# Optimization experiments

Hardware: AMD Instinct MI355X
Metric: run time of the kernel (lower is better)

The kernel has to match this reference:

```python
import jax, jax.numpy as jnp
import numpy as np

N = 100_000      # nodes
E = 1_600_000    # edges (no self loops; reference appends them)
G = 1_000        # graphs
FIN = 27         # input node features
HID = 128        # hidden_channels
L = 4            # num_layers
H = 8            # num_heads
B = 4            # num_bases
A = 3            # aggregators: sum, mean, max
FH = HID // H    # per-head out dim
EPS = 1e-5


def setup_inputs() -> dict:
    key = jax.random.key(0)
    ks = jax.random.split(key, 16)
    s = 0.05
    x = jax.random.normal(ks[0], (N, FIN), jnp.float32)
    src = jax.random.randint(ks[1], (E,), 0, N)
    off = jax.random.randint(ks[2], (E,), 1, N)
    dst = (src + off) % N  # guaranteed no self loops
    edge_index = jnp.stack([src, dst]).astype(jnp.int64)
    batch = jnp.sort(jax.random.randint(ks[3], (N,), 0, G)).astype(jnp.int64)
    return {
        "x": x,
        "lin1_w": jax.random.normal(ks[4], (FIN, HID), jnp.float32) * s,
        "lin1_b": jnp.zeros((HID,), jnp.float32),
        "bn1_g": jnp.ones((HID,), jnp.float32),
        "bn1_b": jnp.zeros((HID,), jnp.float32),
        "bases_w": jax.random.normal(ks[5], (L, HID, B * FH), jnp.float32) * s,
        "comb_w": jax.random.normal(ks[6], (L, HID, H * B * A), jnp.float32) * s,
        "comb_b": jnp.zeros((L, H * B * A), jnp.float32),
        "conv_bias": jnp.zeros((L, HID), jnp.float32),
        "bn_g": jnp.ones((L, HID), jnp.float32),
        "bn_b": jnp.zeros((L, HID), jnp.float32),
        "mlp_w1": jax.random.normal(ks[7], (HID, HID // 2), jnp.float32) * s,
        "mbn1_g": jnp.ones((HID // 2,), jnp.float32),
        "mbn1_b": jnp.zeros((HID // 2,), jnp.float32),
        "mlp_w2": jax.random.normal(ks[8], (HID // 2, HID // 4), jnp.float32) * s,
        "mbn2_g": jnp.ones((HID // 4,), jnp.float32),
        "mbn2_b": jnp.zeros((HID // 4,), jnp.float32),
        "mlp_w3": jax.random.normal(ks[9], (HID // 4, 10), jnp.float32) * s,
        "mlp_b3": jnp.zeros((10,), jnp.float32),
        "edge_index": edge_index,
        "batch": batch,
    }


def _bn(h, g, b):
    # BatchNorm1d, training mode (biased batch variance), per-feature over nodes
    mu = jnp.mean(h, axis=0)
    var = jnp.mean((h - mu) ** 2, axis=0)
    return g * (h - mu) * jax.lax.rsqrt(var + EPS) + b


def reference(x, lin1_w, lin1_b, bn1_g, bn1_b, bases_w, comb_w, comb_b,
              conv_bias, bn_g, bn_b, mlp_w1, mbn1_g, mbn1_b, mlp_w2,
              mbn2_g, mbn2_b, mlp_w3, mlp_b3, edge_index, batch):
    # add self loops (inputs contain none, matching remove+add in EGConv)
    loop = jnp.arange(N, dtype=edge_index.dtype)
    src = jnp.concatenate([edge_index[0], loop])
    dst = jnp.concatenate([edge_index[1], loop])

    h = jax.nn.relu(_bn(x @ lin1_w + lin1_b, bn1_g, bn1_b))  # [N, HID]

    ones_e = jnp.ones((src.shape[0], 1), h.dtype)
    deg = jax.ops.segment_sum(ones_e, dst, num_segments=N)  # [N,1], >=1 via self loops

    for l in range(L):
        bases = h @ bases_w[l]                              # [N, B*FH]
        comb = (h @ comb_w[l] + comb_b[l]).reshape(N, H, A * B)
        msg = bases[src]                                    # [E+N, B*FH]
        ssum = jax.ops.segment_sum(msg, dst, num_segments=N)
        smean = ssum / deg
        smax = jax.ops.segment_max(msg, dst, num_segments=N)
        agg = jnp.stack([ssum, smean, smax], axis=1)        # [N, A, B*FH]
        agg = agg.reshape(N, A * B, FH)
        out = jnp.einsum('nhk,nkf->nhf', comb, agg).reshape(N, HID) + conv_bias[l]
        h = h + jax.nn.relu(_bn(out, bn_g[l], bn_b[l]))

    # global mean pool over graphs
    gsum = jax.ops.segment_sum(h, batch, num_segments=G)
    gcnt = jnp.maximum(jax.ops.segment_sum(jnp.ones((N, 1), h.dtype), batch, num_segments=G), 1.0)
    g = gsum / gcnt                                         # [G, HID]

    g = jax.nn.relu(_bn(g @ mlp_w1, mbn1_g, mbn1_b))
    g = jax.nn.relu(_bn(g @ mlp_w2, mbn2_g, mbn2_b))
    return g @ mlp_w3 + mlp_b3                              # [G, 10]
```

## Files before the change

### kernel.cpp

```cpp
#include <hip/hip_runtime.h>

#define EPSV 1e-5f
#define NEGINF -3.402823466e38f
#define NBMAX 1600
#define CHUNK 8192
#define CAP3 6144

typedef short bf16x8 __attribute__((ext_vector_type(8)));
typedef float f32x4 __attribute__((ext_vector_type(4)));

__device__ __forceinline__ unsigned short f2bf(float f) {
    union { float f; unsigned i; } c; c.f = f;
    unsigned r = c.i + 0x7fff + ((c.i >> 16) & 1);
    return (unsigned short)(r >> 16);
}
__device__ __forceinline__ float blo(unsigned u) {
    union { unsigned i; float f; } c; c.i = u << 16; return c.f;
}
__device__ __forceinline__ float bhi(unsigned u) {
    union { unsigned i; float f; } c; c.i = u & 0xffff0000u; return c.f;
}
__device__ __forceinline__ float bfu(unsigned short u) {
    union { unsigned i; float f; } c; c.i = ((unsigned)u) << 16; return c.f;
}

__global__ __launch_bounds__(256)
void k_lin1(const float* __restrict__ x, const float* __restrict__ w,
            const float* __restrict__ bvec, unsigned short* __restrict__ outb,
            float* __restrict__ stats, int N)
{
    __shared__ float wl[27 * 128];
    int tid = threadIdx.x;
    for (int i = tid; i < 27 * 128; i += 256) wl[i] = w[i];
    __syncthreads();

    int l  = tid & 63;
    int wv = tid >> 6;
    float bv0 = bvec[l], bv1 = bvec[64 + l];
    int waveSlots = gridDim.x * 4;
    int trips = (N + waveSlots - 1) / waveSlots;
    float s0 = 0.f, q0 = 0.f, s1 = 0.f, q1 = 0.f;
    for (int it = 0; it < trips; ++it) {
        int n = (it * gridDim.x + blockIdx.x) * 4 + wv;
        if (n < N) {
            const float* xr = x + (size_t)n * 27;
            float a0 = bv0, a1 = bv1;
            #pragma unroll
            for (int k = 0; k < 27; ++k) {
                float xv = xr[k];
                a0 = fmaf(xv, wl[k * 128 + l], a0);
                a1 = fmaf(xv, wl[k * 128 + 64 + l], a1);
            }
            outb[(size_t)n * 128 + l] = f2bf(a0);
            outb[(size_t)n * 128 + 64 + l] = f2bf(a1);
            s0 += a0; q0 += a0 * a0; s1 += a1; q1 += a1 * a1;
        }
    }
    __shared__ float sred[4][256];
    sred[0][tid] = s0; sred[1][tid] = q0;
    sred[2][tid] = s1; sred[3][tid] = q1;
    __syncthreads();
    if (tid < 64) {
        int t = tid;
        float v0 = sred[0][t] + sred[0][t + 64] + sred[0][t + 128] + sred[0][t + 192];
        float v1 = sred[1][t] + sred[1][t + 64] + sred[1][t + 128] + sred[1][t + 192];
        float v2 = sred[2][t] + sred[2][t + 64] + sred[2][t + 128] + sred[2][t + 192];
        float v3 = sred[3][t] + sred[3][t + 64] + sred[3][t + 128] + sred[3][t + 192];
        atomicAdd(stats + t, v0);
        atomicAdd(stats + 128 + t, v1);
        atomicAdd(stats + 64 + t, v2);
        atomicAdd(stats + 192 + t, v3);
    }
}

__global__ __launch_bounds__(256)
void k_p1_hist(const int* __restrict__ dst, int* __restrict__ bcnt,
               int E, int NB, int shift)
{
    __shared__ int hist[NBMAX];
    for (int i = threadIdx.x; i < NB; i += 256) hist[i] = 0;
    __syncthreads();
    int stride = gridDim.x * 256;
    for (int e = blockIdx.x * 256 + threadIdx.x; e < E; e += stride)
        atomicAdd(&hist[dst[e] >> shift], 1);
    __syncthreads();
    for (int i = threadIdx.x; i < NB; i += 256)
        if (hist[i]) atomicAdd(bcnt + i, hist[i]);
}

__global__ void k_scan1(const int* __restrict__ cnt, int* __restrict__ rowptr,
                        int* __restrict__ bsum, int N)
{
    __shared__ int sb[256];
    int i = blockIdx.x * 256 + threadIdx.x;
    int v = (i < N) ? cnt[i] : 0;
    sb[threadIdx.x] = v;
    __syncthreads();
    for (int ofs = 1; ofs < 256; ofs <<= 1) {
        int u = (threadIdx.x >= ofs) ? sb[threadIdx.x - ofs] : 0;
        __syncthreads();
        sb[threadIdx.x] += u;
        __syncthreads();
    }
    if (i < N) rowptr[i] = sb[threadIdx.x] - v;
    if (threadIdx.x == 255) bsum[blockIdx.x] = sb[255];
}

__global__ void k_scan2(int* __restrict__ bs, int nb)
{
    __shared__ int sb[512];
    int t = threadIdx.x;
    int v = (t < nb) ? bs[t] : 0;
    sb[t] = v;
    __syncthreads();
    for (int ofs = 1; ofs < 512; ofs <<= 1) {
        int u = (t >= ofs) ? sb[t - ofs] : 0;
        __syncthreads();
        sb[t] += u;
        __syncthreads();
    }
    bs[t] = sb[t] - v;
}

__global__ void k_scan3(int* __restrict__ rowptr, const int* __restrict__ bsum,
                        int N, int E)
{
    int i = blockIdx.x * blockDim.x + threadIdx.x;
    if (i < N) rowptr[i] += bsum[i >> 8];
    if (i == 0) rowptr[N] = E;
}

__global__ __launch_bounds__(256)
void k_p2_scatter(const int* __restrict__ src, const int* __restrict__ dst,
                  const int* __restrict__ bbase, int* __restrict__ bcur0,
                  uint2* __restrict__ bucketed, int E, int NB, int shift)
{
    __shared__ uint2 ebuf[CHUNK];
    __shared__ int hist[NBMAX];
    __shared__ int cur[NBMAX];
    __shared__ int wtmp[256];
    int tid = threadIdx.x;
    int c0 = blockIdx.x * CHUNK;
    int cc = min(CHUNK, E - c0);
    if (cc <= 0) return;

    for (int i = tid; i < NB; i += 256) hist[i] = 0;
    __syncthreads();
    for (int i = tid; i < cc; i += 256)
        atomicAdd(&hist[dst[c0 + i] >> shift], 1);
    __syncthreads();
    int per = (NB + 255) / 256;
    int beg = tid * per, end = min(beg + per, NB);
    int s = 0;
    for (int i = beg; i < end; ++i) s += hist[i];
    wtmp[tid] = s;
    __syncthreads();
    for (int ofs = 1; ofs < 256; ofs <<= 1) {
        int u = (tid >= ofs) ? wtmp[tid - ofs] : 0;
        __syncthreads();
        wtmp[tid] += u;
        __syncthreads();
    }
    int run = wtmp[tid] - s;
    for (int i = beg; i < end; ++i) { cur[i] = run; run += hist[i]; }
    __syncthreads();
    for (int i = tid; i < cc; i += 256) {
        int sv = src[c0 + i], dv = dst[c0 + i];
        int b = dv >> shift;
        int pos = atomicAdd(&cur[b], 1);
        ebuf[pos] = make_uint2((unsigned)sv, (unsigned)dv);
    }
    __syncthreads();
    for (int b = tid; b < NB; b += 256) {
        int c = hist[b];
        if (c > 0) {
            int lb = cur[b] - c;
            int gb = bbase[b] + atomicAdd(&bcur0[b], c);
            hist[b] = gb - lb;
        }
    }
    __syncthreads();
    for (int i = tid; i < cc; i += 256) {
        uint2 u = ebuf[i];
        int b = (int)(u.y >> shift);
        bucketed[hist[b] + i] = u;
    }
}

__global__ __launch_bounds__(256)
void k_p3_csr(const uint2* __restrict__ bucketed, const int* __restrict__ bbase,
              int* __restrict__ rowptr, int* __restrict__ csr,
              int N, int NB, int shift)
{
    __shared__ int ncnt[128], nsc[128];
    __shared__ int lcsr[CAP3];
    int b = blockIdx.x;
    int tid = threadIdx.x;
    int e0 = bbase[b], e1 = bbase[b + 1];
    int cnt = e1 - e0;
    int node0 = b << shift;
    int nodes = min(1 << shift, N - node0);

    if (tid < 128) ncnt[tid] = 0;
    __syncthreads();
    for (int i = tid; i < cnt; i += 256)
        atomicAdd(&ncnt[(int)bucketed[e0 + i].y - node0], 1);
    __syncthreads();
    if (tid < 128) nsc[tid] = ncnt[tid];
    __syncthreads();
    for (int ofs = 1; ofs < 128; ofs <<= 1) {
        int u = 0;
        if (tid < 128 && tid >= ofs) u = nsc[tid - ofs];
        __syncthreads();
        if (tid < 128) nsc[tid] += u;
        __syncthreads();
    }
    if (tid < nodes) rowptr[node0 + tid] = e0 + nsc[tid] - ncnt[tid];
    if (tid == 0 && b == NB - 1) rowptr[N] = e1;
    if (tid < 128) ncnt[tid] = nsc[tid] - ncnt[tid];
    __syncthreads();
    if (cnt <= CAP3) {
        for (int i = tid; i < cnt; i += 256) {
            uint2 u = bucketed[e0 + i];
            int d = (int)u.y - node0;
            int pos = atomicAdd(&ncnt[d], 1);
            lcsr[pos] = (int)u.x;
        }
        __syncthreads();
        for (int i = tid; i < cnt; i += 256) csr[e0 + i] = lcsr[i];
    } else {
        for (int i = tid; i < cnt; i += 256) {
            uint2 u = bucketed[e0 + i];
            int d = (int)u.y - node0;
            int pos = atomicAdd(&ncnt[d], 1);
            csr[e0 + pos] = (int)u.x;
        }
    }
}

__global__ __launch_bounds__(256)
void k_gemm_mfma(const unsigned short* __restrict__ tin, unsigned short* __restrict__ h,
                 const float* __restrict__ stats, const float* __restrict__ gamma,
                 const float* __restrict__ beta, float invN, int residual,
                 const float* __restrict__ basesW, const float* __restrict__ combW,
                 const float* __restrict__ combB,
                 unsigned short* __restrict__ basesP,
                 unsigned short* __restrict__ combB16, int N)
{
    __shared__ unsigned short Wlds[2560 * 8];
    __shared__ float scL[128], shL[128];
    int tid = threadIdx.x;
    if (tid < 128) {
        float mu  = stats[tid] * invN;
        float var = stats[128 + tid] * invN - mu * mu;
        float sc  = gamma[tid] * rsqrtf(var + EPSV);
        scL[tid] = sc;
        shL[tid] = beta[tid] - mu * sc;
    }
    for (int i = tid; i < 2560; i += 256) {
        int ct = i >> 8, rem = i & 255;
        int ln = rem & 63;
        int n16 = ln & 15, quad = ln >> 4;
        int k = ((rem >> 6) << 5) + quad * 8;
        unsigned short tmp[8];
        if (ct < 4) {
            int c = ct * 16 + n16;
            #pragma unroll
            for (int j = 0; j < 8; ++j) tmp[j] = f2bf(basesW[(k + j) * 64 + c]);
        } else {
            int c = (ct - 4) * 16 + n16;
            #pragma unroll
            for (int j = 0; j < 8; ++j) tmp[j] = f2bf(combW[(k + j) * 96 + c]);
        }
        uint4 pk;
        pk.x = (unsigned)tmp[0] | ((unsigned)tmp[1] << 16);
        pk.y = (unsigned)tmp[2] | ((unsigned)tmp[3] << 16);
        pk.z = (unsigned)tmp[4] | ((unsigned)tmp[5] << 16);
        pk.w = (unsigned)tmp[6] | ((unsigned)tmp[7] << 16);
        *(uint4*)&Wlds[(size_t)i * 8] = pk;
    }
    __syncthreads();

    int lane = tid & 63, wv = tid >> 6;
    int f = lane & 15, quad = lane >> 4;
    float cbv[6];
    #pragma unroll
    for (int s = 0; s < 6; ++s) cbv[s] = combB[s * 16 + f];

    int tiles = (N + 15) >> 4;
    int waveSlots = gridDim.x * 4;
    for (int tile = blockIdx.x * 4 + wv; tile < tiles; tile += waveSlots) {
        int tb = tile * 16;
        int mnode = min(tb + f, N - 1);
        size_t rbase = (size_t)mnode * 128;

        f32x4 acc[10];
        #pragma unroll
        for (int ct = 0; ct < 10; ++ct) acc[ct] = (f32x4){0.f, 0.f, 0.f, 0.f};

        #pragma unroll
        for (int ki = 0; ki < 4; ++ki) {
            int kc = quad * 8 + ki * 32;
            uint4 tv = *(const uint4*)&tin[rbase + kc];
            float r0, r1, r2, r3, r4, r5, r6, r7;
            r0 = fmaxf(blo(tv.x) * scL[kc]     + shL[kc],     0.f);
            r1 = fmaxf(bhi(tv.x) * scL[kc + 1] + shL[kc + 1], 0.f);
            r2 = fmaxf(blo(tv.y) * scL[kc + 2] + shL[kc + 2], 0.f);
            r3 = fmaxf(bhi(tv.y) * scL[kc + 3] + shL[kc + 3], 0.f);
            r4 = fmaxf(blo(tv.z) * scL[kc + 4] + shL[kc + 4], 0.f);
            r5 = fmaxf(bhi(tv.z) * scL[kc + 5] + shL[kc + 5], 0.f);
            r6 = fmaxf(blo(tv.w) * scL[kc + 6] + shL[kc + 6], 0.f);
            r7 = fmaxf(bhi(tv.w) * scL[kc + 7] + shL[kc + 7], 0.f);
            if (residual) {
                uint4 hv = *(const uint4*)&h[rbase + kc];
                r0 += blo(hv.x); r1 += bhi(hv.x); r2 += blo(hv.y); r3 += bhi(hv.y);
                r4 += blo(hv.z); r5 += bhi(hv.z); r6 += blo(hv.w); r7 += bhi(hv.w);
            }
            unsigned short b0 = f2bf(r0), b1 = f2bf(r1), b2 = f2bf(r2), b3 = f2bf(r3);
            unsigned short b4 = f2bf(r4), b5 = f2bf(r5), b6 = f2bf(r6), b7 = f2bf(r7);
            uint4 hw;
            hw.x = (unsigned)b0 | ((unsigned)b1 << 16);
            hw.y = (unsigned)b2 | ((unsigned)b3 << 16);
            hw.z = (unsigned)b4 | ((unsigned)b5 << 16);
            hw.w = (unsigned)b6 | ((unsigned)b7 << 16);
            *(uint4*)&h[rbase + kc] = hw;
            short ab[8] = {(short)b0, (short)b1, (short)b2, (short)b3,
                           (short)b4, (short)b5, (short)b6, (short)b7};
            bf16x8 a = *(bf16x8*)ab;
            #pragma unroll
            for (int ct = 0; ct < 10; ++ct) {
                bf16x8 bfr = *(const bf16x8*)&Wlds[(size_t)((ct * 4 + ki) * 64 + lane) * 8];
                acc[ct] = __builtin_amdgcn_mfma_f32_16x16x32_bf16(a, bfr, acc[ct], 0, 0, 0);
            }
        }

        #pragma unroll
        for (int r = 0; r < 4; ++r) {
            int node = tb + quad * 4 + r;
            if (node < N) {
                #pragma unroll
                for (int ct = 0; ct < 4; ++ct)
                    basesP[(size_t)node * 64 + f * 4 + ct] = f2bf(acc[ct][r]);
                #pragma unroll
                for (int s = 0; s < 6; ++s)
                    combB16[(size_t)node * 96 + s * 16 + f] = f2bf(acc[4 + s][r] + cbv[s]);
            }
        }
    }
}

__global__ __launch_bounds__(256)
void k_agg(const unsigned short* __restrict__ basesP, const unsigned short* __restrict__ combB16,
           const int* __restrict__ csr, const int* __restrict__ rowptr,
           const float* __restrict__ cbias, unsigned short* __restrict__ outb,
           float* __restrict__ stats, int N)
{
    int l = threadIdx.x & 63;
    int w = threadIdx.x >> 6;
    int f = l & 15, sub = l >> 4;
    const char* bp = (const char*)basesP;
    unsigned fof = (unsigned)(f << 3);
    float cb0 = cbias[l], cb1 = cbias[64 + l];
    int waveSlots = gridDim.x * 4;
    int pairs = (N + 1) >> 1;
    int trips = (pairs + waveSlots - 1) / waveSlots;
    float s0 = 0.f, q0 = 0.f, s1 = 0.f, q1 = 0.f;

    for (int it = 0; it < trips; ++it) {
        int pr = (it * gridDim.x + blockIdx.x) * 4 + w;
        if (pr < pairs) {
            int nA = pr * 2;
            bool hasB = (nA + 1) < N;
            int nB = hasB ? nA + 1 : nA;
            int rA = rowptr[nA];
            int cA = rowptr[nA + 1] - rA;
            int rB = rowptr[nB];
            int cB = hasB ? (rowptr[nB + 1] - rB) : 0;

            float SA0 = 0.f, SA1 = 0.f, SA2 = 0.f, SA3 = 0.f;
            float MA0 = NEGINF, MA1 = NEGINF, MA2 = NEGINF, MA3 = NEGINF;
            float SB0 = 0.f, SB1 = 0.f, SB2 = 0.f, SB3 = 0.f;
            float MB0 = NEGINF, MB1 = NEGINF, MB2 = NEGINF, MB3 = NEGINF;

            int mt = (max(cA, cB) + 3) >> 2;
            int e = sub;
            #pragma unroll 2
            for (int t = 0; t < mt; ++t) {
                int eA = max(min(e, cA - 1), 0);
                int eB = max(min(e, cB - 1), 0);
                int snA = csr[rA + eA];
                int snB = csr[rB + eB];
                uint2 uA = *(const uint2*)(bp + (((unsigned)snA) << 7) + fof);
                uint2 uB = *(const uint2*)(bp + (((unsigned)snB) << 7) + fof);
                bool vA = e < cA, vB = e < cB;
                float a0 = blo(uA.x), a1 = bhi(uA.x), a2 = blo(uA.y), a3 = bhi(uA.y);
                float b0 = blo(uB.x), b1 = bhi(uB.x), b2 = blo(uB.y), b3 = bhi(uB.y);
                SA0 += vA ? a0 : 0.f; SA1 += vA ? a1 : 0.f;
                SA2 += vA ? a2 : 0.f; SA3 += vA ? a3 : 0.f;
                MA0 = fmaxf(MA0, vA ? a0 : NEGINF); MA1 = fmaxf(MA1, vA ? a1 : NEGINF);
                MA2 = fmaxf(MA2, vA ? a2 : NEGINF); MA3 = fmaxf(MA3, vA ? a3 : NEGINF);
                SB0 += vB ? b0 : 0.f; SB1 += vB ? b1 : 0.f;
                SB2 += vB ? b2 : 0.f; SB3 += vB ? b3 : 0.f;
                MB0 = fmaxf(MB0, vB ? b0 : NEGINF); MB1 = fmaxf(MB1, vB ? b1 : NEGINF);
                MB2 = fmaxf(MB2, vB ? b2 : NEGINF); MB3 = fmaxf(MB3, vB ? b3 : NEGINF);
                e += 4;
            }

            {
                float T0 = SA0, T1 = SA1, T2 = SA2, T3 = SA3;
                float X0 = MA0, X1 = MA1, X2 = MA2, X3 = MA3;
                T0 += __shfl_xor(T0, 16, 64); T1 += __shfl_xor(T1, 16, 64);
                T2 += __shfl_xor(T2, 16, 64); T3 += __shfl_xor(T3, 16, 64);
                T0 += __shfl_xor(T0, 32, 64); T1 += __shfl_xor(T1, 32, 64);
                T2 += __shfl_xor(T2, 32, 64); T3 += __shfl_xor(T3, 32, 64);
                X0 = fmaxf(X0, __shfl_xor(X0, 16, 64)); X1 = fmaxf(X1, __shfl_xor(X1, 16, 64));
                X2 = fmaxf(X2, __shfl_xor(X2, 16, 64)); X3 = fmaxf(X3, __shfl_xor(X3, 16, 64));
                X0 = fmaxf(X0, __shfl_xor(X0, 32, 64)); X1 = fmaxf(X1, __shfl_xor(X1, 32, 64));
                X2 = fmaxf(X2, __shfl_xor(X2, 32, 64)); X3 = fmaxf(X3, __shfl_xor(X3, 32, 64));
                uint2 su = *(const uint2*)(bp + (((unsigned)nA) << 7) + fof);
                float w0 = blo(su.x), w1 = bhi(su.x), w2 = blo(su.y), w3 = bhi(su.y);
                T0 += w0; T1 += w1; T2 += w2; T3 += w3;
                X0 = fmaxf(X0, w0); X1 = fmaxf(X1, w1);
                X2 = fmaxf(X2, w2); X3 = fmaxf(X3, w3);
                float invd = 1.f / (float)(cA + 1);
                float A0 = T0 * invd, A1 = T1 * invd, A2 = T2 * invd, A3 = T3 * invd;

                const unsigned short* cr = combB16 + (size_t)nA * 96;
                const uint2* c0p = (const uint2*)(cr + sub * 12);
                const uint2* c1p = (const uint2*)(cr + 48 + sub * 12);
                uint2 qa0 = c0p[0], qa1 = c0p[1], qa2 = c0p[2];
                uint2 qb0 = c1p[0], qb1 = c1p[1], qb2 = c1p[2];

                float o0 = cb0, o1 = cb1;
                o0 = fmaf(blo(qa0.x), T0, o0); o0 = fmaf(bhi(qa0.x), T1, o0);
                o0 = fmaf(blo(qa0.y), T2, o0); o0 = fmaf(bhi(qa0.y), T3, o0);
                o0 = fmaf(blo(qa1.x), A0, o0); o0 = fmaf(bhi(qa1.x), A1, o0);
                o0 = fmaf(blo(qa1.y), A2, o0); o0 = fmaf(bhi(qa1.y), A3, o0);
                o0 = fmaf(blo(qa2.x), X0, o0); o0 = fmaf(bhi(qa2.x), X1, o0);
                o0 = fmaf(blo(qa2.y), X2, o0); o0 = fmaf(bhi(qa2.y), X3, o0);
                o1 = fmaf(blo(qb0.x), T0, o1); o1 = fmaf(bhi(qb0.x), T1, o1);
                o1 = fmaf(blo(qb0.y), T2, o1); o1 = fmaf(bhi(qb0.y), T3, o1);
                o1 = fmaf(blo(qb1.x), A0, o1); o1 = fmaf(bhi(qb1.x), A1, o1);
                o1 = fmaf(blo(qb1.y), A2, o1); o1 = fmaf(bhi(qb1.y), A3, o1);
                o1 = fmaf(blo(qb2.x), X0, o1); o1 = fmaf(bhi(qb2.x), X1, o1);
                o1 = fmaf(blo(qb2.y), X2, o1); o1 = fmaf(bhi(qb2.y), X3, o1);

                outb[(size_t)nA * 128 + l] = f2bf(o0);
                outb[(size_t)nA * 128 + 64 + l] = f2bf(o1);
                s0 += o0; q0 += o0 * o0; s1 += o1; q1 += o1 * o1;
            }
            if (hasB) {
                float T0 = SB0, T1 = SB1, T2 = SB2, T3 = SB3;
                float X0 = MB0, X1 = MB1, X2 = MB2, X3 = MB3;
                T0 += __shfl_xor(T0, 16, 64); T1 += __shfl_xor(T1, 16, 64);
                T2 += __shfl_xor(T2, 16, 64); T3 += __shfl_xor(T3, 16, 64);
                T0 += __shfl_xor(T0, 32, 64); T1 += __shfl_xor(T1, 32, 64);
                T2 += __shfl_xor(T2, 32, 64); T3 += __shfl_xor(T3, 32, 64);
                X0 = fmaxf(X0, __shfl_xor(X0, 16, 64)); X1 = fmaxf(X1, __shfl_xor(X1, 16, 64));
                X2 = fmaxf(X2, __shfl_xor(X2, 16, 64)); X3 = fmaxf(X3, __shfl_xor(X3, 16, 64));
                X0 = fmaxf(X0, __shfl_xor(X0, 32, 64)); X1 = fmaxf(X1, __shfl_xor(X1, 32, 64));
                X2 = fmaxf(X2, __shfl_xor(X2, 32, 64)); X3 = fmaxf(X3, __shfl_xor(X3, 32, 64));
                uint2 su = *(const uint2*)(bp + (((unsigned)nB) << 7) + fof);
                float w0 = blo(su.x), w1 = bhi(su.x), w2 = blo(su.y), w3 = bhi(su.y);
                T0 += w0; T1 += w1; T2 += w2; T3 += w3;
                X0 = fmaxf(X0, w0); X1 = fmaxf(X1, w1);
                X2 = fmaxf(X2, w2); X3 = fmaxf(X3, w3);
                float invd = 1.f / (float)(cB + 1);
                float A0 = T0 * invd, A1 = T1 * invd, A2 = T2 * invd, A3 = T3 * invd;

                const unsigned short* cr = combB16 + (size_t)nB * 96;
                const uint2* c0p = (const uint2*)(cr + sub * 12);
                const uint2* c1p = (const uint2*)(cr + 48 + sub * 12);
                uint2 qa0 = c0p[0], qa1 = c0p[1], qa2 = c0p[2];
                uint2 qb0 = c1p[0], qb1 = c1p[1], qb2 = c1p[2];

                float o0 = cb0, o1 = cb1;
                o0 = fmaf(blo(qa0.x), T0, o0); o0 = fmaf(bhi(qa0.x), T1, o0);
                o0 = fmaf(blo(qa0.y), T2, o0); o0 = fmaf(bhi(qa0.y), T3, o0);
                o0 = fmaf(blo(qa1.x), A0, o0); o0 = fmaf(bhi(qa1.x), A1, o0);
                o0 = fmaf(blo(qa1.y), A2, o0); o0 = fmaf(bhi(qa1.y), A3, o0);
                o0 = fmaf(blo(qa2.x), X0, o0); o0 = fmaf(bhi(qa2.x), X1, o0);
                o0 = fmaf(blo(qa2.y), X2, o0); o0 = fmaf(bhi(qa2.y), X3, o0);
                o1 = fmaf(blo(qb0.x), T0, o1); o1 = fmaf(bhi(qb0.x), T1, o1);
                o1 = fmaf(blo(qb0.y), T2, o1); o1 = fmaf(bhi(qb0.y), T3, o1);
                o1 = fmaf(blo(qb1.x), A0, o1); o1 = fmaf(bhi(qb1.x), A1, o1);
                o1 = fmaf(blo(qb1.y), A2, o1); o1 = fmaf(bhi(qb1.y), A3, o1);
                o1 = fmaf(blo(qb2.x), X0, o1); o1 = fmaf(bhi(qb2.x), X1, o1);
                o1 = fmaf(blo(qb2.y), X2, o1); o1 = fmaf(bhi(qb2.y), X3, o1);

                outb[(size_t)nB * 128 + l] = f2bf(o0);
                outb[(size_t)nB * 128 + 64 + l] = f2bf(o1);
                s0 += o0; q0 += o0 * o0; s1 += o1; q1 += o1 * o1;
            }
        }
    }
    __shared__ float sred[4][256];
    sred[0][threadIdx.x] = s0; sred[1][threadIdx.x] = q0;
    sred[2][threadIdx.x] = s1; sred[3][threadIdx.x] = q1;
    __syncthreads();
    if (threadIdx.x < 64) {
        int t = threadIdx.x;
        float v0 = sred[0][t] + sred[0][t + 64] + sred[0][t + 128] + sred[0][t + 192];
        float v1 = sred[1][t] + sred[1][t + 64] + sred[1][t + 128] + sred[1][t + 192];
        float v2 = sred[2][t] + sred[2][t + 64] + sred[2][t + 128] + sred[2][t + 192];
        float v3 = sred[3][t] + sred[3][t + 64] + sred[3][t + 128] + sred[3][t + 192];
        atomicAdd(stats + t, v0);
        atomicAdd(stats + 128 + t, v1);
        atomicAdd(stats + 64 + t, v2);
        atomicAdd(stats + 192 + t, v3);
    }
}

__global__ void k_gbound(const int* __restrict__ batch, int* __restrict__ gstart,
                         int N, int G)
{
    int stride = gridDim.x * blockDim.x;
    for (int n = blockIdx.x * blockDim.x + threadIdx.x; n < N; n += stride) {
        int b = batch[n];
        if (n == 0) {
            for (int g = 0; g <= b; ++g) gstart[g] = 0;
        } else {
            int pb = batch[n - 1];
            for (int g = pb + 1; g <= b; ++g) gstart[g] = n;
        }
        if (n == N - 1) {
            for (int g = b + 1; g <= G; ++g) gstart[g] = N;
        }
    }
}

__global__ __launch_bounds__(256)
void k_gmean(const unsigned short* __restrict__ t, const unsigned short* __restrict__ h,
             const float* __restrict__ stats, const float* __restrict__ gamma,
             const float* __restrict__ beta, float invN,
             const int* __restrict__ gstart, float* __restrict__ gout, int G)
{
    __shared__ float part[128];
    int g = blockIdx.x;
    if (g >= G) return;
    int c = threadIdx.x & 127;
    int half = threadIdx.x >> 7;
    float mu  = stats[c] * invN;
    float var = stats[128 + c] * invN - mu * mu;
    float sc  = gamma[c] * rsqrtf(var + EPSV);
    float sh  = beta[c] - mu * sc;
    int s = gstart[g], e = gstart[g + 1];
    float acc = 0.f;
    #pragma unroll 2
    for (int n = s + half; n < e; n += 2) {
        size_t o = (size_t)n * 128 + c;
        acc += bfu(h[o]) + fmaxf(bfu(t[o]) * sc + sh, 0.f);
    }
    if (half) part[c] = acc;
    __syncthreads();
    if (!half) {
        float tot = acc + part[c];
        float cntf = fmaxf((float)(e - s), 1.f);
        gout[g * 128 + c] = tot / cntf;
    }
}

__global__ void k_mlp1(const float* __restrict__ gin, const float* __restrict__ w1,
                       float* __restrict__ t1, float* __restrict__ stats, int G)
{
    int g = blockIdx.x;
    int c = threadIdx.x;
    const float* gr = gin + g * 128;
    float acc = 0.f;
    for (int k = 0; k < 128; ++k) acc = fmaf(gr[k], w1[k * 64 + c], acc);
    t1[g * 64 + c] = acc;
    atomicAdd(stats + c, acc);
    atomicAdd(stats + 64 + c, acc * acc);
}

__global__ void k_mlp2(const float* __restrict__ t1, const float* __restrict__ stats1,
                       const float* __restrict__ g1, const float* __restrict__ b1,
                       const float* __restrict__ w2, float* __restrict__ t2,
                       float* __restrict__ stats2, float invG, int G)
{
    __shared__ float row[64];
    int g = blockIdx.x;
    int c = threadIdx.x;
    float v = t1[g * 64 + c];
    float mu = stats1[c] * invG;
    float var = stats1[64 + c] * invG - mu * mu;
    row[c] = fmaxf(g1[c] * (v - mu) * rsqrtf(var + EPSV) + b1[c], 0.f);
    __syncthreads();
    if (c < 32) {
        float acc = 0.f;
        #pragma unroll
        for (int k = 0; k < 64; ++k) acc = fmaf(row[k], w2[k * 32 + c], acc);
        t2[g * 32 + c] = acc;
        atomicAdd(stats2 + c, acc);
        atomicAdd(stats2 + 32 + c, acc * acc);
    }
}

__global__ void k_mlp3(const float* __restrict__ t2, const float* __restrict__ stats2,
                       const float* __restrict__ g2, const float* __restrict__ b2,
                       const float* __restrict__ w3, const float* __restrict__ b3,
                       float* __restrict__ out, float invG, int G)
{
    __shared__ float row[32];
    int g = blockIdx.x;
    int c = threadIdx.x;
    if (c < 32) {
        float v = t2[g * 32 + c];
        float mu = stats2[c] * invG;
        float var = stats2[32 + c] * invG - mu * mu;
        row[c] = fmaxf(g2[c] * (v - mu) * rsqrtf(var + EPSV) + b2[c], 0.f);
    }
    __syncthreads();
    if (c < 10) {
        float acc = b3[c];
        #pragma unroll
        for (int k = 0; k < 32; ++k) acc = fmaf(row[k], w3[k * 10 + c], acc);
        out[g * 10 + c] = acc;
    }
}

extern "C" void kernel_launch(void* const* d_in, const int* in_sizes, int n_in,
                              void* d_out, int out_size, void* d_ws, size_t ws_size,
                              hipStream_t stream)
{
    const float* x        = (const float*)d_in[0];
    const float* lin1_w   = (const float*)d_in[1];
    const float* lin1_b   = (const float*)d_in[2];
    const float* bn1_g    = (const float*)d_in[3];
    const float* bn1_b    = (const float*)d_in[4];
    const float* bases_w  = (const float*)d_in[5];
    const float* comb_w   = (const float*)d_in[6];
    const float* comb_b   = (const float*)d_in[7];
    const float* conv_bias= (const float*)d_in[8];
    const float* bn_g     = (const float*)d_in[9];
    const float* bn_b     = (const float*)d_in[10];
    const float* mlp_w1   = (const float*)d_in[11];
    const float* mbn1_g   = (const float*)d_in[12];
    const float* mbn1_b   = (const float*)d_in[13];
    const float* mlp_w2   = (const float*)d_in[14];
    const float* mbn2_g   = (const float*)d_in[15];
    const float* mbn2_b   = (const float*)d_in[16];
    const float* mlp_w3   = (const float*)d_in[17];
    const float* mlp_b3   = (const float*)d_in[18];
    const int*   edge_idx = (const int*)d_in[19];
    const int*   batch    = (const int*)d_in[20];
    float* outp = (float*)d_out;

    const int N = in_sizes[20];
    const int E = in_sizes[19] / 2;
    const int G = out_size / 10;
    const int* esrc = edge_idx;
    const int* edst = edge_idx + E;

    int shift = 6;
    while ((((N - 1) >> shift) + 1) > NBMAX && shift < 7) ++shift;
    const int NB = ((N - 1) >> shift) + 1;

    char* p = (char*)d_ws;
    auto alloc = [&](size_t bytes) {
        char* r = p;
        p += (bytes + 255) & ~(size_t)255;
        return r;
    };
    unsigned short* h      = (unsigned short*)alloc((size_t)N * 128 * 2);
    unsigned short* basesP = (unsigned short*)alloc((size_t)N * 64 * 2);
    unsigned short* combB16= (unsigned short*)alloc((size_t)N * 96 * 2);
    unsigned short* outb   = (unsigned short*)alloc((size_t)N * 128 * 2);
    int*            csr    = (int*)  alloc((size_t)(E + 64) * 4);
    int*            rowptr = (int*)  alloc((size_t)(N + 1) * 4);
    int*            bbase  = (int*)  alloc((size_t)(NB + 1) * 4);
    float*          tg     = (float*)alloc((size_t)G * 128 * 4);
    float*          t1     = (float*)alloc((size_t)G * 64 * 4);
    float*          t2     = (float*)alloc((size_t)G * 32 * 4);
    int*            gstart = (int*)  alloc((size_t)(G + 1) * 4);
    int*            bsum   = (int*)  alloc(512 * 4);
    char*           zbase  = p;
    int*            bcnt   = (int*)  alloc((size_t)NB * 4);
    int*            bcur0  = (int*)  alloc((size_t)NB * 4);
    float*          stats  = (float*)alloc(7 * 256 * 4);
    size_t zbytes = (size_t)(p - zbase);
    uint2* bucketed = (uint2*)combB16;
    (void)ws_size; (void)n_in;

    hipMemsetAsync(zbase, 0, zbytes, stream);

    const float invN = 1.0f / (float)N;
    const float invG = 1.0f / (float)G;
    const int nbB = (NB + 255) / 256;

    k_lin1<<<1024, 256, 0, stream>>>(x, lin1_w, lin1_b, outb, stats, N);
    k_p1_hist<<<256, 256, 0, stream>>>(edst, bcnt, E, NB, shift);
    k_scan1<<<nbB, 256, 0, stream>>>(bcnt, bbase, bsum, NB);
    k_scan2<<<1, 512, 0, stream>>>(bsum, nbB);
    k_scan3<<<nbB, 256, 0, stream>>>(bbase, bsum, NB, E);
    k_p2_scatter<<<(E + CHUNK - 1) / CHUNK, 256, 0, stream>>>(esrc, edst, bbase, bcur0,
                                                              bucketed, E, NB, shift);
    k_p3_csr<<<NB, 256, 0, stream>>>(bucketed, bbase, rowptr, csr, N, NB, shift);

    for (int l = 0; l < 4; ++l) {
        const float* bw = bases_w + (size_t)l * 128 * 64;
        const float* cw = comb_w + (size_t)l * 128 * 96;
        const float* cb = comb_b + (size_t)l * 96;
        const float* cvb = conv_bias + (size_t)l * 128;
        const float* pg = (l == 0) ? bn1_g : bn_g + (l - 1) * 128;
        const float* pb = (l == 0) ? bn1_b : bn_b + (l - 1) * 128;
        k_gemm_mfma<<<512, 256, 0, stream>>>(outb, h, stats + l * 256, pg, pb, invN,
                                             l > 0 ? 1 : 0, bw, cw, cb, basesP, combB16, N);
        k_agg<<<2048, 256, 0, stream>>>(basesP, combB16, csr, rowptr, cvb,
                                        outb, stats + (1 + l) * 256, N);
    }

    k_gbound<<<512, 256, 0, stream>>>(batch, gstart, N, G);
    k_gmean<<<G, 256, 0, stream>>>(outb, h, stats + 4 * 256, bn_g + 3 * 128,
                                   bn_b + 3 * 128, invN, gstart, tg, G);
    float* st5 = stats + 5 * 256;
    float* st6 = stats + 6 * 256;
    k_mlp1<<<G, 64, 0, stream>>>(tg, mlp_w1, t1, st5, G);
    k_mlp2<<<G, 64, 0, stream>>>(t1, st5, mbn1_g, mbn1_b, mlp_w2, t2, st6, invG, G);
    k_mlp3<<<G, 64, 0, stream>>>(t2, st6, mbn2_g, mbn2_b, mlp_w3, mlp_b3, outp, invG, G);
}
```

Measured before the change: 778.7 us.

## Fuse histogram+scan+graph-bounds and pooling+MLP tail into last-block kernels

Merges the bucket histogram, the three-kernel scan and the graph-boundary computation into one launch, where the last histogram block to arrive (detected with an atomic counter) performs the exclusive scan. Likewise fuses graph mean pooling and the three MLP/BN stages into one kernel, with the last-arriving block doing the batch-norm-dependent MLP layers 2 and 3 serially. The aggregation kernel's duplicated A/B epilogue is folded into an unrolled loop. This removes about seven kernel launches and their gaps, but puts the tail MLP work on a single block and relies on threadfence/atomic last-block ordering.

Result: slower. 982.5 us (+26.2%).

```diff
diff --git a/kernel.cpp b/kernel.cpp
--- a/kernel.cpp
+++ b/kernel.cpp
@@ -74,60 +74,67 @@
 }
 
 __global__ __launch_bounds__(256)
-void k_p1_hist(const int* __restrict__ dst, int* __restrict__ bcnt,
-               int E, int NB, int shift)
-{
+void k_prep(const int* __restrict__ dst, int* __restrict__ bcnt, int* __restrict__ bbase,
+            int E, int NB, int shift, const int* __restrict__ batch,
+            int* __restrict__ gstart, int N, int G, int* __restrict__ arrive)
+{
+    const int HB = 256;
+    int tid = threadIdx.x;
     __shared__ int hist[NBMAX];
-    for (int i = threadIdx.x; i < NB; i += 256) hist[i] = 0;
-    __syncthreads();
-    int stride = gridDim.x * 256;
-    for (int e = blockIdx.x * 256 + threadIdx.x; e < E; e += stride)
-        atomicAdd(&hist[dst[e] >> shift], 1);
-    __syncthreads();
-    for (int i = threadIdx.x; i < NB; i += 256)
-        if (hist[i]) atomicAdd(bcnt + i, hist[i]);
-}
-
-__global__ void k_scan1(const int* __restrict__ cnt, int* __restrict__ rowptr,
-                        int* __restrict__ bsum, int N)
-{
-    __shared__ int sb[256];
-    int i = blockIdx.x * 256 + threadIdx.x;
-    int v = (i < N) ? cnt[i] : 0;
-    sb[threadIdx.x] = v;
-    __syncthreads();
-    for (int ofs = 1; ofs < 256; ofs <<= 1) {
-        int u = (threadIdx.x >= ofs) ? sb[threadIdx.x - ofs] : 0;
-        __syncthreads();
-        sb[threadIdx.x] += u;
-        __syncthreads();
-    }
-    if (i < N) rowptr[i] = sb[threadIdx.x] - v;
-    if (threadIdx.x == 255) bsum[blockIdx.x] = sb[255];
-}
-
-__global__ void k_scan2(int* __restrict__ bs, int nb)
-{
-    __shared__ int sb[512];
-    int t = threadIdx.x;
-    int v = (t < nb) ? bs[t] : 0;
-    sb[t] = v;
-    __syncthreads();
-    for (int ofs = 1; ofs < 512; ofs <<= 1) {
-        int u = (t >= ofs) ? sb[t - ofs] : 0;
-        __syncthreads();
-        sb[t] += u;
-        __syncthreads();
-    }
-    bs[t] = sb[t] - v;
-}
-
-__global__ void k_scan3(int* __restrict__ rowptr, const int* __restrict__ bsum,
-                        int N, int E)
-{
-    int i = blockIdx.x * blockDim.x + threadIdx.x;
-    if (i < N) rowptr[i] += bsum[i >> 8];
-    if (i == 0) rowptr[N] = E;
+    __shared__ int buf2[NBMAX];
+    __shared__ int partl[256];
+    __shared__ int lastf;
+
+    if (blockIdx.x < HB) {
+        for (int i = tid; i < NB; i += 256) hist[i] = 0;
+        __syncthreads();
+        int stride = HB * 256;
+        for (int e = blockIdx.x * 256 + tid; e < E; e += stride)
+            atomicAdd(&hist[dst[e] >> shift], 1);
+        __syncthreads();
+        for (int i = tid; i < NB; i += 256)
+            if (hist[i]) atomicAdd(bcnt + i, hist[i]);
+        __syncthreads();
+        if (tid == 0) {
+            __threadfence();
+            int tk = atomicAdd(arrive, 1);
+            lastf = (tk == HB - 1) ? 1 : 0;
+        }
+        __syncthreads();
+        if (lastf) {
+            __threadfence();
+            int per = (NB + 255) / 256;
+            int beg = tid * per, end = min(beg + per, NB);
+            int s = 0;
+            for (int i = beg; i < end; ++i) { int v = bcnt[i]; buf2[i] = s; s += v; }
+            partl[tid] = s;
+            __syncthreads();
+            for (int ofs = 1; ofs < 256; ofs <<= 1) {
+                int u = (tid >= ofs) ? partl[tid - ofs] : 0;
+                __syncthreads();
+                partl[tid] += u;
+                __syncthreads();
+            }
+            int add = partl[tid] - s;
+            for (int i = beg; i < end; ++i) bbase[i] = buf2[i] + add;
+            if (tid == 0) bbase[NB] = E;
+        }
+    } else {
+        int b = blockIdx.x - HB;
+        int stride = (gridDim.x - HB) * 256;
+        for (int n = b * 256 + tid; n < N; n += stride) {
+            int bb = batch[n];
+            if (n == 0) {
+                for (int g = 0; g <= bb; ++g) gstart[g] = 0;
+            } else {
+                int pb = batch[n - 1];
+                for (int g = pb + 1; g <= bb; ++g) gstart[g] = n;
+            }
+            if (n == N - 1) {
+                for (int g = bb + 1; g <= G; ++g) gstart[g] = N;
+            }
+        }
+    }
 }
 
 __global__ __launch_bounds__(256)
@@ -406,9 +413,15 @@
                 e += 4;
             }
 
-            {
-                float T0 = SA0, T1 = SA1, T2 = SA2, T3 = SA3;
-                float X0 = MA0, X1 = MA1, X2 = MA2, X3 = MA3;
+            #pragma unroll
+            for (int m = 0; m < 2; ++m) {
+                if (m == 1 && !hasB) break;
+                int n = (m == 0) ? nA : nB;
+                int cnt = (m == 0) ? cA : cB;
+                float T0 = (m == 0) ? SA0 : SB0, T1 = (m == 0) ? SA1 : SB1;
+                float T2 = (m == 0) ? SA2 : SB2, T3 = (m == 0) ? SA3 : SB3;
+                float X0 = (m == 0) ? MA0 : MB0, X1 = (m == 0) ? MA1 : MB1;
+                float X2 = (m == 0) ? MA2 : MB2, X3 = (m == 0) ? MA3 : MB3;
                 T0 += __shfl_xor(T0, 16, 64); T1 += __shfl_xor(T1, 16, 64);
                 T2 += __shfl_xor(T2, 16, 64); T3 += __shfl_xor(T3, 16, 64);
                 T0 += __shfl_xor(T0, 32, 64); T1 += __shfl_xor(T1, 32, 64);
@@ -417,15 +430,15 @@
                 X2 = fmaxf(X2, __shfl_xor(X2, 16, 64)); X3 = fmaxf(X3, __shfl_xor(X3, 16, 64));
                 X0 = fmaxf(X0, __shfl_xor(X0, 32, 64)); X1 = fmaxf(X1, __shfl_xor(X1, 32, 64));
                 X2 = fmaxf(X2, __shfl_xor(X2, 32, 64)); X3 = fmaxf(X3, __shfl_xor(X3, 32, 64));
-                uint2 su = *(const uint2*)(bp + (((unsigned)nA) << 7) + fof);
+                uint2 su = *(const uint2*)(bp + (((unsigned)n) << 7) + fof);
                 float w0 = blo(su.x), w1 = bhi(su.x), w2 = blo(su.y), w3 = bhi(su.y);
                 T0 += w0; T1 += w1; T2 += w2; T3 += w3;
                 X0 = fmaxf(X0, w0); X1 = fmaxf(X1, w1);
                 X2 = fmaxf(X2, w2); X3 = fmaxf(X3, w3);
-                float invd = 1.f / (float)(cA + 1);
+                float invd = 1.f / (float)(cnt + 1);
                 float A0 = T0 * invd, A1 = T1 * invd, A2 = T2 * invd, A3 = T3 * invd;
 
-                const unsigned short* cr = combB16 + (size_t)nA * 96;
+                const unsigned short* cr = combB16 + (size_t)n * 96;
                 const uint2* c0p = (const uint2*)(cr + sub * 12);
                 const uint2* c1p = (const uint2*)(cr + 48 + sub * 12);
                 uint2 qa0 = c0p[0], qa1 = c0p[1], qa2 = c0p[2];
@@ -445,51 +458,8 @@
                 o1 = fmaf(blo(qb2.x), X0, o1); o1 = fmaf(bhi(qb2.x), X1, o1);
                 o1 = fmaf(blo(qb2.y), X2, o1); o1 = fmaf(bhi(qb2.y), X3, o1);
 
-                outb[(size_t)nA * 128 + l] = f2bf(o0);
-                outb[(size_t)nA * 128 + 64 + l] = f2bf(o1);
-                s0 += o0; q0 += o0 * o0; s1 += o1; q1 += o1 * o1;
-            }
-            if (hasB) {
-                float T0 = SB0, T1 = SB1, T2 = SB2, T3 = SB3;
-                float X0 = MB0, X1 = MB1, X2 = MB2, X3 = MB3;
-                T0 += __shfl_xor(T0, 16, 64); T1 += __shfl_xor(T1, 16, 64);
-                T2 += __shfl_xor(T2, 16, 64); T3 += __shfl_xor(T3, 16, 64);
-                T0 += __shfl_xor(T0, 32, 64); T1 += __shfl_xor(T1, 32, 64);
-                T2 += __shfl_xor(T2, 32, 64); T3 += __shfl_xor(T3, 32, 64);
-                X0 = fmaxf(X0, __shfl_xor(X0, 16, 64)); X1 = fmaxf(X1, __shfl_xor(X1, 16, 64));
-                X2 = fmaxf(X2, __shfl_xor(X2, 16, 64)); X3 = fmaxf(X3, __shfl_xor(X3, 16, 64));
-                X0 = fmaxf(X0, __shfl_xor(X0, 32, 64)); X1 = fmaxf(X1, __shfl_xor(X1, 32, 64));
-                X2 = fmaxf(X2, __shfl_xor(X2, 32, 64)); X3 = fmaxf(X3, __shfl_xor(X3, 32, 64));
-                uint2 su = *(const uint2*)(bp + (((unsigned)nB) << 7) + fof);
-                float w0 = blo(su.x), w1 = bhi(su.x), w2 = blo(su.y), w3 = bhi(su.y);
-                T0 += w0; T1 += w1; T2 += w2; T3 += w3;
-                X0 = fmaxf(X0, w0); X1 = fmaxf(X1, w1);
-                X2 = fmaxf(X2, w2); X3 = fmaxf(X3, w3);
-                float invd = 1.f / (float)(cB + 1);
-                float A0 = T0 * invd, A1 = T1 * invd, A2 = T2 * invd, A3 = T3 * invd;
-
-                const unsigned short* cr = combB16 + (size_t)nB * 96;
-                const uint2* c0p = (const uint2*)(cr + sub * 12);
-                const uint2* c1p = (const uint2*)(cr + 48 + sub * 12);
-                uint2 qa0 = c0p[0], qa1 = c0p[1], qa2 = c0p[2];
-                uint2 qb0 = c1p[0], qb1 = c1p[1], qb2 = c1p[2];
-
-                float o0 = cb0, o1 = cb1;
-                o0 = fmaf(blo(qa0.x), T0, o0); o0 = fmaf(bhi(qa0.x), T1, o0);
-                o0 = fmaf(blo(qa0.y), T2, o0); o0 = fmaf(bhi(qa0.y), T3, o0);
-                o0 = fmaf(blo(qa1.x), A0, o0); o0 = fmaf(bhi(qa1.x), A1, o0);
-                o0 = fmaf(blo(qa1.y), A2, o0); o0 = fmaf(bhi(qa1.y), A3, o0);
-                o0 = fmaf(blo(qa2.x), X0, o0); o0 = fmaf(bhi(qa2.x), X1, o0);
-                o0 = fmaf(blo(qa2.y), X2, o0); o0 = fmaf(bhi(qa2.y), X3, o0);
-                o1 = fmaf(blo(qb0.x), T0, o1); o1 = fmaf(bhi(qb0.x), T1, o1);
-                o1 = fmaf(blo(qb0.y), T2, o1); o1 = fmaf(bhi(qb0.y), T3, o1);
-                o1 = fmaf(blo(qb1.x), A0, o1); o1 = fmaf(bhi(qb1.x), A1, o1);
-                o1 = fmaf(blo(qb1.y), A2, o1); o1 = fmaf(bhi(qb1.y), A3, o1);
-                o1 = fmaf(blo(qb2.x), X0, o1); o1 = fmaf(bhi(qb2.x), X1, o1);
-                o1 = fmaf(blo(qb2.y), X2, o1); o1 = fmaf(bhi(qb2.y), X3, o1);
-
-                outb[(size_t)nB * 128 + l] = f2bf(o0);
-                outb[(size_t)nB * 128 + 64 + l] = f2bf(o1);
+                outb[(size_t)n * 128 + l] = f2bf(o0);
+                outb[(size_t)n * 128 + 64 + l] = f2bf(o1);
                 s0 += o0; q0 += o0 * o0; s1 += o1; q1 += o1 * o1;
             }
         }
@@ -511,111 +481,111 @@
     }
 }
 
-__global__ void k_gbound(const int* __restrict__ batch, int* __restrict__ gstart,
-                         int N, int G)
-{
-    int stride = gridDim.x * blockDim.x;
-    for (int n = blockIdx.x * blockDim.x + threadIdx.x; n < N; n += stride) {
-        int b = batch[n];
-        if (n == 0) {
-            for (int g = 0; g <= b; ++g) gstart[g] = 0;
-        } else {
-            int pb = batch[n - 1];
-            for (int g = pb + 1; g <= b; ++g) gstart[g] = n;
-        }
-        if (n == N - 1) {
-            for (int g = b + 1; g <= G; ++g) gstart[g] = N;
-        }
-    }
-}
-
 __global__ __launch_bounds__(256)
-void k_gmean(const unsigned short* __restrict__ t, const unsigned short* __restrict__ h,
-             const float* __restrict__ stats, const float* __restrict__ gamma,
-             const float* __restrict__ beta, float invN,
-             const int* __restrict__ gstart, float* __restrict__ gout, int G)
-{
+void k_tail(const unsigned short* __restrict__ t, const unsigned short* __restrict__ h,
+            const float* __restrict__ stats4, const float* __restrict__ gamma,
+            const float* __restrict__ beta, float invN, const int* __restrict__ gstart,
+            const float* __restrict__ w1, float* __restrict__ t1, float* __restrict__ st5,
+            const float* __restrict__ g1, const float* __restrict__ b1,
+            const float* __restrict__ w2, float* __restrict__ t2,
+            const float* __restrict__ g2, const float* __restrict__ b2,
+            const float* __restrict__ w3, const float* __restrict__ b3,
+            float* __restrict__ out, float invG, int G, int* __restrict__ arrive)
+{
+    __shared__ float tg[128];
     __shared__ float part[128];
+    __shared__ float red[4][64];
+    __shared__ int lastf;
+    __shared__ float sc1[64], sh1[64], s6[64];
+    __shared__ float sc2[32], sh2[32];
+
     int g = blockIdx.x;
-    if (g >= G) return;
-    int c = threadIdx.x & 127;
-    int half = threadIdx.x >> 7;
-    float mu  = stats[c] * invN;
-    float var = stats[128 + c] * invN - mu * mu;
-    float sc  = gamma[c] * rsqrtf(var + EPSV);
-    float sh  = beta[c] - mu * sc;
-    int s = gstart[g], e = gstart[g + 1];
-    float acc = 0.f;
-    #pragma unroll 2
-    for (int n = s + half; n < e; n += 2) {
-        size_t o = (size_t)n * 128 + c;
-        acc += bfu(h[o]) + fmaxf(bfu(t[o]) * sc + sh, 0.f);
-    }
-    if (half) part[c] = acc;
-    __syncthreads();
-    if (!half) {
-        float tot = acc + part[c];
-        float cntf = fmaxf((float)(e - s), 1.f);
-        gout[g * 128 + c] = tot / cntf;
-    }
-}
-
-__global__ void k_mlp1(const float* __restrict__ gin, const float* __restrict__ w1,
-                       float* __restrict__ t1, float* __restrict__ stats, int G)
-{
-    int g = blockIdx.x;
-    int c = threadIdx.x;
-    const float* gr = gin + g * 128;
-    float acc = 0.f;
-    for (int k = 0; k < 128; ++k) acc = fmaf(gr[k], w1[k * 64 + c], acc);
-    t1[g * 64 + c] = acc;
-    atomicAdd(stats + c, acc);
-    atomicAdd(stats + 64 + c, acc * acc);
-}
-
-__global__ void k_mlp2(const float* __restrict__ t1, const float* __restrict__ stats1,
-                       const float* __restrict__ g1, const float* __restrict__ b1,
-                       const float* __restrict__ w2, float* __restrict__ t2,
-                       float* __restrict__ stats2, float invG, int G)
-{
-    __shared__ float row[64];
-    int g = blockIdx.x;
-    int c = threadIdx.x;
-    float v = t1[g * 64 + c];
-    float mu = stats1[c] * invG;
-    float var = stats1[64 + c] * invG - mu * mu;
-    row[c] = fmaxf(g1[c] * (v - mu) * rsqrtf(var + EPSV) + b1[c], 0.f);
-    __syncthreads();
-    if (c < 32) {
+    int tid = threadIdx.x;
+    {
+        int c = tid & 127, half = tid >> 7;
+        float mu  = stats4[c] * invN;
+        float var = stats4[128 + c] * invN - mu * mu;
+        float sc  = gamma[c] * rsqrtf(var + EPSV);
+        float sh  = beta[c] - mu * sc;
+        int s = gstart[g], e = gstart[g + 1];
         float acc = 0.f;
+        #pragma unroll 2
+        for (int n = s + half; n < e; n += 2) {
+            size_t o = (size_t)n * 128 + c;
+            acc += bfu(h[o]) + fmaxf(bfu(t[o]) * sc + sh, 0.f);
+        }
+        if (half) part[c] = acc;
+        __syncthreads();
+        if (!half) tg[c] = (acc + part[c]) / fmaxf((float)(e - s), 1.f);
+        __syncthreads();
+    }
+    {
+        int cc = tid & 63, pp = tid >> 6;
+        float a = 0.f;
+        int k0 = pp * 32;
         #pragma unroll
-        for (int k = 0; k < 64; ++k) acc = fmaf(row[k], w2[k * 32 + c], acc);
-        t2[g * 32 + c] = acc;
-        atomicAdd(stats2 + c, acc);
-        atomicAdd(stats2 + 32 + c, acc * acc);
-    }
-}
-
-__global__ void k_mlp3(const float* __restrict__ t2, const float* __restrict__ stats2,
-                       const float* __restrict__ g2, const float* __restrict__ b2,
-                       const float* __restrict__ w3, const float* __restrict__ b3,
-                       float* __restrict__ out, float invG, int G)
-{
-    __shared__ float row[32];
-    int g = blockIdx.x;
-    int c = threadIdx.x;
-    if (c < 32) {
-        float v = t2[g * 32 + c];
-        float mu = stats2[c] * invG;
-        float var = stats2[32 + c] * invG - mu * mu;
-        row[c] = fmaxf(g2[c] * (v - mu) * rsqrtf(var + EPSV) + b2[c], 0.f);
-    }
-    __syncthreads();
-    if (c < 10) {
-        float acc = b3[c];
-        #pragma unroll
-        for (int k = 0; k < 32; ++k) acc = fmaf(row[k], w3[k * 10 + c], acc);
-        out[g * 10 + c] = acc;
+        for (int k = 0; k < 32; ++k)
+            a = fmaf(tg[k0 + k], w1[(k0 + k) * 64 + cc], a);
+        red[pp][cc] = a;
+        __syncthreads();
+        if (tid < 64) {
+            float v = red[0][tid] + red[1][tid] + red[2][tid] + red[3][tid];
+            t1[g * 64 + tid] = v;
+            atomicAdd(st5 + tid, v);
+            atomicAdd(st5 + 64 + tid, v * v);
+        }
+    }
+    if (tid == 0) {
+        __threadfence();
+        int tk = atomicAdd(arrive, 1);
+        lastf = (tk == G - 1) ? 1 : 0;
+    }
+    __syncthreads();
+    if (!lastf) return;
+    __threadfence();
+    if (tid < 64) {
+        float m  = st5[tid] * invG;
+        float vv = st5[64 + tid] * invG - m * m;
+        float s_ = g1[tid] * rsqrtf(vv + EPSV);
+        sc1[tid] = s_;
+        sh1[tid] = b1[tid] - m * s_;
+        s6[tid] = 0.f;
+    }
+    __syncthreads();
+    {
+        int cc = tid & 31, gofs = tid >> 5;
+        float sacc = 0.f, qacc = 0.f;
+        for (int gg = gofs; gg < G; gg += 8) {
+            float a = 0.f;
+            #pragma unroll 8
+            for (int k = 0; k < 64; ++k) {
+                float rv = fmaxf(t1[gg * 64 + k] * sc1[k] + sh1[k], 0.f);
+                a = fmaf(rv, w2[k * 32 + cc], a);
+            }
+            t2[gg * 32 + cc] = a;
+            sacc += a; qacc += a * a;
+        }
+        atomicAdd(&s6[cc], sacc);
+        atomicAdd(&s6[32 + cc], qacc);
+    }
+    __syncthreads();
+    if (tid < 32) {
+        float m  = s6[tid] * invG;
+        float vv = s6[32 + tid] * invG - m * m;
+        float s_ = g2[tid] * rsqrtf(vv + EPSV);
+        sc2[tid] = s_;
+        sh2[tid] = b2[tid] - m * s_;
+    }
+    __syncthreads();
+    for (int idx = tid; idx < G * 10; idx += 256) {
+        int gg = idx / 10, cc = idx - gg * 10;
+        float a = b3[cc];
+        #pragma unroll 8
+        for (int k = 0; k < 32; ++k) {
+            float rv = fmaxf(t2[gg * 32 + k] * sc2[k] + sh2[k], 0.f);
+            a = fmaf(rv, w3[k * 10 + cc], a);
+        }
+        out[idx] = a;
     }
 }
 
@@ -669,15 +639,14 @@
     int*            csr    = (int*)  alloc((size_t)(E + 64) * 4);
     int*            rowptr = (int*)  alloc((size_t)(N + 1) * 4);
     int*            bbase  = (int*)  alloc((size_t)(NB + 1) * 4);
-    float*          tg     = (float*)alloc((size_t)G * 128 * 4);
     float*          t1     = (float*)alloc((size_t)G * 64 * 4);
     float*          t2     = (float*)alloc((size_t)G * 32 * 4);
     int*            gstart = (int*)  alloc((size_t)(G + 1) * 4);
-    int*            bsum   = (int*)  alloc(512 * 4);
     char*           zbase  = p;
     int*            bcnt   = (int*)  alloc((size_t)NB * 4);
     int*            bcur0  = (int*)  alloc((size_t)NB * 4);
     float*          stats  = (float*)alloc(7 * 256 * 4);
+    int*            arrive = (int*)  alloc(2 * 4);
     size_t zbytes = (size_t)(p - zbase);
     uint2* bucketed = (uint2*)combB16;
     (void)ws_size; (void)n_in;
@@ -686,13 +655,10 @@
 
     const float invN = 1.0f / (float)N;
     const float invG = 1.0f / (float)G;
-    const int nbB = (NB + 255) / 256;
 
     k_lin1<<<1024, 256, 0, stream>>>(x, lin1_w, lin1_b, outb, stats, N);
-    k_p1_hist<<<256, 256, 0, stream>>>(edst, bcnt, E, NB, shift);
-    k_scan1<<<nbB, 256, 0, stream>>>(bcnt, bbase, bsum, NB);
-    k_scan2<<<1, 512, 0, stream>>>(bsum, nbB);
-    k_scan3<<<nbB, 256, 0, stream>>>(bbase, bsum, NB, E);
+    k_prep<<<768, 256, 0, stream>>>(edst, bcnt, bbase, E, NB, shift,
+                                    batch, gstart, N, G, arrive);
     k_p2_scatter<<<(E + CHUNK - 1) / CHUNK, 256, 0, stream>>>(esrc, edst, bbase, bcur0,
                                                               bucketed, E, NB, shift);
     k_p3_csr<<<NB, 256, 0, stream>>>(bucketed, bbase, rowptr, csr, N, NB, shift);
@@ -710,12 +676,10 @@
                                         outb, stats + (1 + l) * 256, N);
     }
 
-    k_gbound<<<512, 256, 0, stream>>>(batch, gstart, N, G);
-    k_gmean<<<G, 256, 0, stream>>>(outb, h, stats + 4 * 256, bn_g + 3 * 128,
-                                   bn_b + 3 * 128, invN, gstart, tg, G);
-    float* st5 = stats + 5 * 256;
-    float* st6 = stats + 6 * 256;
-    k_mlp1<<<G, 64, 0, stream>>>(tg, mlp_w1, t1, st5, G);
-    k_mlp2<<<G, 64, 0, stream>>>(t1, st5, mbn1_g, mbn1_b, mlp_w2, t2, st6, invG, G);
-    k_mlp3<<<G, 64, 0, stream>>>(t2, st6, mbn2_g, mbn2_b, mlp_w3, mlp_b3, outp, invG, G);
-}
+    k_tail<<<G, 256, 0, stream>>>(outb, h, stats + 4 * 256, bn_g + 3 * 128,
+                                  bn_b + 3 * 128, invN, gstart,
+                                  mlp_w1, t1, stats + 5 * 256,
+                                  mbn1_g, mbn1_b, mlp_w2, t2,
+                                  mbn2_g, mbn2_b, mlp_w3, mlp_b3,
+                                  outp, invG, G, arrive + 1);
+}
```
